# Kernel tuning notes

Hardware: AMD Instinct MI355X
Metric: run time of the kernel (lower is better)

Reference implementation:

```python
import jax, jax.numpy as jnp
import numpy as np

ATOM_K = 10
VOX_K = 15
HEADS = 4
HEAD_DIM = 32
N_BLOCKS = 4
BLOCK_DEPTH = 2


def _pairwise_sqdist(a, b):
    # a: [Na,3], b: [Nb,3] -> [Na,Nb]
    return jnp.sum(a * a, 1)[:, None] + jnp.sum(b * b, 1)[None, :] - 2.0 * (a @ b.T)


def knn(src_pos, dst_pos, k):
    # for each dst point, k nearest src points; returns (dst_idx, src_idx), each [Nd*k]
    d2 = _pairwise_sqdist(dst_pos, src_pos)
    _, idx = jax.lax.top_k(-d2, k)
    dst = jnp.repeat(jnp.arange(dst_pos.shape[0]), k)
    return dst, idx.reshape(-1)


def knn_graph(pos, k):
    # k nearest neighbors excluding self; returns (src=neighbor, dst=center)
    n = pos.shape[0]
    d2 = _pairwise_sqdist(pos, pos) + jnp.eye(n, dtype=pos.dtype) * 1e10
    _, idx = jax.lax.top_k(-d2, k)
    dst = jnp.repeat(jnp.arange(n), k)
    return idx.reshape(-1), dst


def edge_weights(i0, i1, h_a, pos_a, h_b, pos_b, w1, b1, w2, b2):
    # MLP([2*A+1, 8, 1]) on concat(h_a[i0], h_b[i1], dist) -> scalar per edge
    d = jnp.sqrt(jnp.sum((pos_a[i0] - pos_b[i1]) ** 2, -1, keepdims=True) + 1e-12)
    feat = jnp.concatenate([h_a[i0], h_b[i1], d], -1)
    return (jax.nn.relu(feat @ w1 + b1) @ w2 + b2)[:, 0]


def attn_layer(h, src, dst, ew, wq_l, wk_l, wv_l, n):
    # edge-weighted multi-head graph attention with segment softmax over dst
    q = (h @ wq_l).reshape(n, HEADS, HEAD_DIM)
    k = (h @ wk_l).reshape(n, HEADS, HEAD_DIM)
    v = (h @ wv_l).reshape(n, HEADS, HEAD_DIM)
    logits = jnp.sum(q[dst] * k[src], -1) / jnp.sqrt(jnp.float32(HEAD_DIM)) + ew[:, None]  # [E,H]
    m = jax.ops.segment_max(logits, dst, num_segments=n)
    z = jnp.exp(logits - m[dst])
    s = jax.ops.segment_sum(z, dst, num_segments=n)
    alpha = z / (s[dst] + 1e-9)
    out = jax.ops.segment_sum(alpha[:, :, None] * v[src], dst, num_segments=n)
    return out.reshape(n, HEADS * HEAD_DIM)


def layer_norm(x, g, b):
    mu = jnp.mean(x, -1, keepdims=True)
    var = jnp.var(x, -1, keepdims=True)
    return (x - mu) * jax.lax.rsqrt(var + 1e-5) * g + b


def setup_inputs() -> dict:
    Na, Nv, F, A, OUT = 8192, 4096, 64, 128, 128
    L = N_BLOCKS * BLOCK_DEPTH
    key = jax.random.key(0)
    ks = jax.random.split(key, 20)
    p = lambda k, shape, s=0.05: jax.random.normal(k, shape, jnp.float32) * s
    return {
        'atom_x': jax.random.normal(ks[0], (Na, F), jnp.float32),
        'atom_pos': jax.random.normal(ks[1], (Na, 3), jnp.float32) * 10.0,
        'vox_x': jax.random.normal(ks[2], (Nv, F), jnp.float32),
        'vox_pos': jax.random.normal(ks[3], (Nv, 3), jnp.float32) * 10.0,
        'w_atom_in': p(ks[4], (F, A)), 'b_atom_in': jnp.zeros((A,), jnp.float32),
        'w_vox_in': p(ks[5], (F, A)), 'b_vox_in': jnp.zeros((A,), jnp.float32),
        'aa_w1': p(ks[6], (2 * A + 1, 8)), 'aa_b1': jnp.zeros((8,), jnp.float32),
        'aa_w2': p(ks[7], (8, 1)), 'aa_b2': jnp.zeros((1,), jnp.float32),
        'av_w1': p(ks[8], (2 * A + 1, 8)), 'av_b1': jnp.zeros((8,), jnp.float32),
        'av_w2': p(ks[9], (8, 1)), 'av_b2': jnp.zeros((1,), jnp.float32),
        'vv_w1': p(ks[10], (2 * A + 1, 8)), 'vv_b1': jnp.zeros((8,), jnp.float32),
        'vv_w2': p(ks[11], (8, 1)), 'vv_b2': jnp.zeros((1,), jnp.float32),
        'wq': p(ks[12], (L, A, A)), 'wk': p(ks[13], (L, A, A)), 'wv': p(ks[14], (L, A, A)),
        'ln_g': jnp.ones((L, A), jnp.float32), 'ln_b': jnp.zeros((L, A), jnp.float32),
        'w_o1': p(ks[15], ((N_BLOCKS + 1) * A, A)), 'b_o1': jnp.zeros((A,), jnp.float32),
        'w_o2': p(ks[16], (A, OUT)), 'b_o2': jnp.zeros((OUT,), jnp.float32),
    }


def reference(atom_x, atom_pos, vox_x, vox_pos, w_atom_in, b_atom_in, w_vox_in, b_vox_in,
              aa_w1, aa_b1, aa_w2, aa_b2, av_w1, av_b1, av_w2, av_b2, vv_w1, vv_b1, vv_w2, vv_b2,
              wq, wk, wv, ln_g, ln_b, w_o1, b_o1, w_o2, b_o2):
    Na, Nv = atom_x.shape[0], vox_x.shape[0]
    N = Na + Nv
    atom_h0 = atom_x @ w_atom_in + b_atom_in
    vox_h0 = vox_x @ w_vox_in + b_vox_in

    # multi-scale KNN graph construction
    aa_src, aa_dst = knn_graph(atom_pos, ATOM_K)
    aa_ew = edge_weights(aa_src, aa_dst, atom_h0, atom_pos, atom_h0, atom_pos, aa_w1, aa_b1, aa_w2, aa_b2)
    av_vox, av_atom = knn(atom_pos, vox_pos, VOX_K)  # dst=vox, src=atom
    av_ew = edge_weights(av_vox, av_atom, vox_h0, vox_pos, atom_h0, atom_pos, av_w1, av_b1, av_w2, av_b2)
    vv_src, vv_dst = knn_graph(vox_pos, VOX_K)
    vv_ew = edge_weights(vv_src, vv_dst, vox_h0, vox_pos, vox_h0, vox_pos, vv_w1, vv_b1, vv_w2, vv_b2)

    # combined atom|vox graph (vox nodes offset by Na)
    src = jnp.concatenate([aa_src, av_atom, vv_src + Na])
    dst = jnp.concatenate([aa_dst, av_vox + Na, vv_dst + Na])
    ew = jnp.concatenate([aa_ew, av_ew, vv_ew])
    h = jnp.concatenate([atom_h0, vox_h0], 0)

    block_outs = []
    for b_i in range(N_BLOCKS):
        for l in range(BLOCK_DEPTH):
            li = b_i * BLOCK_DEPTH + l
            h = layer_norm(h + attn_layer(h, src, dst, ew, wq[li], wk[li], wv[li], N), ln_g[li], ln_b[li])
        block_outs.append(h[Na:])

    feat = jnp.concatenate([vox_h0] + block_outs, -1)  # [Nv, (blocks+1)*A]
    return jax.nn.relu(feat @ w_o1 + b_o1) @ w_o2 + b_o2
```

## Files before the change

kernel.cpp:

```cpp
#include <hip/hip_runtime.h>
#include <hip/hip_bf16.h>

#define PE_NA 8192
#define PE_NV 4096
#define PE_NN (PE_NA+PE_NV)
#define PE_FA 128
#define PE_FIN 64
#define PE_KAA 10
#define PE_KAV 15
#define PE_KVV 15
#define PE_EAA (PE_NA*PE_KAA)
#define PE_EAV (PE_NV*PE_KAV)
#define PE_EVV (PE_NV*PE_KVV)
#define PE_ETOT (PE_EAA+PE_EAV+PE_EVV)
#define PE_KNN_BLOCKS (PE_NA/4 + PE_NV/4 + PE_NV/4)
#define PE_P1A 0
#define PE_P2A 65536
#define PE_P2AV 131072
#define PE_P1AV 196608
#define PE_P1V 229376
#define PE_P2V 262144
#define PE_PTOT 294912
#define PE_PRE_BLOCKS (PE_PTOT/256)
#define PE_WT_ELEMS (8*3*128*128)
#define PE_WT_BLOCKS (PE_WT_ELEMS/256)
#define PE_RANK_S 32

typedef __hip_bfloat16 bf16;
typedef __attribute__((ext_vector_type(4))) float f32x4;
typedef __attribute__((ext_vector_type(4))) unsigned int u32x4;
typedef __attribute__((ext_vector_type(8))) short s16x8;
union pe_frag { u32x4 u; s16x8 s; };

__device__ __forceinline__ float pe_b2f(bf16 x){ return __bfloat162float(x); }

__device__ __forceinline__ float pe_u2f(unsigned short u){ return __uint_as_float(((unsigned)u) << 16); }
__device__ __forceinline__ unsigned short pe_f2u(float f){
  unsigned u = __float_as_uint(f);
  u = u + 0x7FFFu + ((u >> 16) & 1u);
  return (unsigned short)(u >> 16);
}

__global__ __launch_bounds__(1024) void pe_probe_kernel(const unsigned short* __restrict__ buf, int n,
                                                        int* __restrict__ flag){
  __shared__ int red[16];
  int t = threadIdx.x;
  int cnt = 0;
  for (int i = t; i < n; i += 1024){
    unsigned u = buf[i];
    unsigned e = (u >> 7) & 0xFF;
    if (u == 0u || (e >= 100u && e <= 150u)) cnt++;
  }
  #pragma unroll
  for (int off = 32; off > 0; off >>= 1) cnt += __shfl_xor(cnt, off);
  if ((t & 63) == 0) red[t >> 6] = cnt;
  __syncthreads();
  if (t == 0){
    int s = 0;
    #pragma unroll
    for (int i = 0; i < 16; i++) s += red[i];
    flag[0] = (s > (n * 9) / 10) ? 0 : 1;
  }
}

struct PeConv {
  const void* src[29];
  long long dstOff[29];
  int n[29];
  int blk0[30];
};
__global__ __launch_bounds__(256) void pe_convall_kernel(PeConv a, float* __restrict__ wsbase,
                                                         const int* __restrict__ flag){
  int b = blockIdx.x;
  int s = 0;
  while (s < 28 && b >= a.blk0[s+1]) s++;
  int idx = (b - a.blk0[s])*256 + threadIdx.x;
  if (idx >= a.n[s]) return;
  float* dst = wsbase + a.dstOff[s];
  if (flag[0]) dst[idx] = ((const float*)a.src[s])[idx];
  else         dst[idx] = pe_b2f(((const bf16*)a.src[s])[idx]);
}

__global__ __launch_bounds__(256) void ProteinEncoder_558345749244_kernel(bf16* __restrict__ out, int n){
  int idx = blockIdx.x*256 + threadIdx.x;
  if (idx < n) out[idx] = __float2bfloat16(0.123f);
}

__global__ __launch_bounds__(256) void pe_packproj_kernel(
    const float* __restrict__ ax, const float* __restrict__ wai, const float* __restrict__ bai,
    const float* __restrict__ vx, const float* __restrict__ wvi, const float* __restrict__ bvi,
    const float* __restrict__ apos, const float* __restrict__ vpos,
    const float* __restrict__ wq, const float* __restrict__ wk, const float* __restrict__ wv,
    float* __restrict__ h, float* __restrict__ voxh0,
    float4* __restrict__ apos4, float4* __restrict__ vpos4,
    int* __restrict__ arank, int* __restrict__ vrank,
    unsigned short* __restrict__ wtb){
  int b = blockIdx.x;
  const int NBA = (PE_NA*PE_FA)/256;
  const int NBV = (PE_NV*PE_FA)/256;
  const int NBP = (PE_NN + 255)/256;
  if (b < NBA){
    int idx = b*256 + threadIdx.x;
    int row = idx >> 7, col = idx & 127;
    const float* xr = ax + row*PE_FIN;
    float acc = bai[col];
    #pragma unroll 8
    for (int k2 = 0; k2 < PE_FIN; k2++) acc += xr[k2] * wai[k2*PE_FA + col];
    h[idx] = acc;
  } else if (b < NBA + NBV){
    int idx = (b - NBA)*256 + threadIdx.x;
    int row = idx >> 7, col = idx & 127;
    const float* xr = vx + row*PE_FIN;
    float acc = bvi[col];
    #pragma unroll 8
    for (int k2 = 0; k2 < PE_FIN; k2++) acc += xr[k2] * wvi[k2*PE_FA + col];
    h[(size_t)PE_NA*PE_FA + idx] = acc;
    voxh0[idx] = acc;
  } else if (b < NBA + NBV + NBP){
    int idx = (b - NBA - NBV)*256 + threadIdx.x;
    if (idx < PE_NA){
      float bx = apos[idx*3+0], by = apos[idx*3+1], bz = apos[idx*3+2];
      apos4[idx] = make_float4(bx, by, bz, (bx*bx + by*by) + bz*bz);
      arank[idx] = 0;
    } else if (idx < PE_NA + PE_NV){
      int j = idx - PE_NA;
      float bx = vpos[j*3+0], by = vpos[j*3+1], bz = vpos[j*3+2];
      vpos4[j] = make_float4(bx, by, bz, (bx*bx + by*by) + bz*bz);
      vrank[j] = 0;
    }
  } else {
    int g = (b - NBA - NBV - NBP)*256 + threadIdx.x;
    int c = g >> 14;
    int r = g & 16383;
    int n = r >> 7, k = r & 127;
    int li = c / 3, mat = c - li*3;
    const float* wsrc = (mat == 0) ? wq : (mat == 1) ? wk : wv;
    wtb[g] = pe_f2u(wsrc[li*16384 + k*128 + n]);
  }
}

__global__ __launch_bounds__(256) void pe_rank_kernel(
    const float4* __restrict__ apos4, const float4* __restrict__ vpos4,
    int* __restrict__ arank, int* __restrict__ vrank){
  __shared__ float xs[256];
  int b = blockIdx.x;
  const int ABLK = (PE_NA/256)*PE_RANK_S;
  const float4* src; int N; int* drk; int cb;
  if (b < ABLK){ src = apos4; N = PE_NA; drk = arank; cb = b; }
  else         { src = vpos4; N = PE_NV; drk = vrank; cb = b - ABLK; }
  int chunk = cb / PE_RANK_S;
  int seg   = cb % PE_RANK_S;
  int i = chunk*256 + threadIdx.x;
  float xi = src[i].x;
  int segN = N / PE_RANK_S;
  int j0 = seg * segN;
  if (threadIdx.x < segN) xs[threadIdx.x] = src[j0 + threadIdx.x].x;
  __syncthreads();
  int cnt = 0;
  #pragma unroll 8
  for (int j = 0; j < segN; j++){
    float xj = xs[j];
    cnt += (xj < xi || (xj == xi && (j0 + j) < i)) ? 1 : 0;
  }
  atomicAdd(&drk[i], cnt);
}

__global__ __launch_bounds__(256) void pe_scatter_kernel(
    const float4* __restrict__ apos4, const float4* __restrict__ vpos4,
    const int* __restrict__ arank, const int* __restrict__ vrank,
    float4* __restrict__ sax4, int* __restrict__ said,
    float4* __restrict__ svx4, int* __restrict__ svid){
  int g = blockIdx.x*256 + threadIdx.x;
  if (g < PE_NA){
    int r = arank[g];
    sax4[r] = apos4[g];
    said[r] = g;
  } else if (g < PE_NN){
    int j = g - PE_NA;
    int r = vrank[j];
    svx4[r] = vpos4[j];
    svid[r] = j;
  }
}

__device__ __forceinline__ float pe_unflip(unsigned th){
  return __uint_as_float(th ^ ((unsigned)(~((int)th >> 31)) | 0x80000000u));
}
__device__ __forceinline__ void pe_knn_insert(unsigned long long mask, float d2, int j,
                                              int K, int lane,
                                              unsigned long long &slot, float &thr_f){
  while (mask){
    int l = __ffsll((long long)mask) - 1;
    mask &= mask - 1;
    float dl = __shfl(d2, l, 64);
    int jl = __shfl(j, l, 64);
    unsigned u = __float_as_uint(dl);
    u ^= (unsigned)(((int)u >> 31) | 0x80000000);
    unsigned long long k = ((unsigned long long)u << 32) | (unsigned)jl;
    unsigned long long skm1 = __shfl(slot, K-1, 64);
    if (k < skm1){
      unsigned long long up = __shfl_up(slot, 1, 64);
      slot = (slot < k) ? slot : ((lane == 0 || up < k) ? k : up);
      thr_f = pe_unflip((unsigned)(__shfl(slot, K-1, 64) >> 32));
    }
  }
}

__global__ __launch_bounds__(256) void pe_knn3_kernel(
    const float4* __restrict__ apos4, const float4* __restrict__ vpos4,
    const float4* __restrict__ sax4, const int* __restrict__ said, const int* __restrict__ arank,
    const float4* __restrict__ svx4, const int* __restrict__ svid, const int* __restrict__ vrank,
    int* __restrict__ es,
    const float* __restrict__ h,
    const float* __restrict__ aw1, const float* __restrict__ vw1, const float* __restrict__ ww1,
    float* __restrict__ Pall){
  int b = blockIdx.x;
  if (b >= PE_KNN_BLOCKS){
    int g = (b - PE_KNN_BLOCKS)*256 + threadIdx.x;
    const float* w1; const float* hb; int n; int half;
    if (g < PE_P2A)       { w1 = aw1; hb = h;                        n = g >> 3;               half = 0; }
    else if (g < PE_P2AV) { w1 = aw1; hb = h;                        n = (g - PE_P2A) >> 3;    half = 1; }
    else if (g < PE_P1AV) { w1 = vw1; hb = h;                        n = (g - PE_P2AV) >> 3;   half = 1; }
    else if (g < PE_P1V)  { w1 = vw1; hb = h + (size_t)PE_NA*PE_FA;  n = (g - PE_P1AV) >> 3;   half = 0; }
    else if (g < PE_P2V)  { w1 = ww1; hb = h + (size_t)PE_NA*PE_FA;  n = (g - PE_P1V) >> 3;    half = 0; }
    else                  { w1 = ww1; hb = h + (size_t)PE_NA*PE_FA;  n = (g - PE_P2V) >> 3;    half = 1; }
    int j = g & 7;
    const float* hr = hb + n*PE_FA;
    const float* wr = w1 + half*128*8 + j;
    float acc = 0.f;
    #pragma unroll 8
    for (int f = 0; f < 128; f++) acc += hr[f] * wr[f*8];
    Pall[g] = acc;
    return;
  }
  const float4 *dpos, *spos; const int *sid, *srank; int Ns, K, excl, idx_off, nb; int* out;
  if (b < PE_NA/4){
    dpos = apos4; spos = sax4; sid = said; srank = arank;
    Ns = PE_NA; K = PE_KAA; excl = 1; idx_off = 0; out = es; nb = b;
  } else if (b < PE_NA/4 + PE_NV/4){
    dpos = vpos4; spos = sax4; sid = said; srank = nullptr;
    Ns = PE_NA; K = PE_KAV; excl = 0; idx_off = 0; out = es + PE_EAA; nb = b - PE_NA/4;
  } else {
    dpos = vpos4; spos = svx4; sid = svid; srank = vrank;
    Ns = PE_NV; K = PE_KVV; excl = 1; idx_off = PE_NA;
    out = es + PE_EAA + PE_EAV; nb = b - PE_NA/4 - PE_NV/4;
  }
  int lane = threadIdx.x & 63;
  int n = nb*4 + (threadIdx.x >> 6);
  float4 dp = dpos[n];
  float qx = dp.x, qy = dp.y, qz = dp.z, nq = dp.w;
  int self = excl ? n : -1;
  int start;
  if (srank){
    start = srank[n];
  } else {
    int lo = 0, len = Ns;
    #pragma unroll
    for (int it = 0; it < 2; it++){
      int step = (len + 63) >> 6;
      int pr = lo + lane*step; if (pr > Ns-1) pr = Ns-1;
      float px = spos[pr].x;
      unsigned long long mv = __ballot(px <= qx);
      int cnt = __popcll(mv);
      int seg = cnt > 0 ? cnt - 1 : 0;
      lo = lo + seg*step;
      len = step;
      if (lo > Ns-1) lo = Ns-1;
    }
    start = lo;
  }
  int w0 = start - 32; if (w0 < 0) w0 = 0; if (w0 > Ns - 64) w0 = Ns - 64;
  unsigned long long slot;
  float thr_f;
  {
    int j = w0 + lane;
    float4 pp = spos[j];
    int oi = sid[j];
    float dt = (qx*pp.x + qy*pp.y) + qz*pp.z;
    float d2 = __builtin_fmaf(-2.0f, dt, nq + pp.w);
    unsigned u = __float_as_uint(d2);
    u ^= (unsigned)(((int)u >> 31) | 0x80000000);
    if (oi == self) u = 0xffffffffu;
    unsigned long long key = ((unsigned long long)u << 32) | (unsigned)oi;
    #pragma unroll
    for (int kk = 2; kk <= 64; kk <<= 1){
      #pragma unroll
      for (int jj = kk >> 1; jj > 0; jj >>= 1){
        unsigned long long o = __shfl_xor(key, jj, 64);
        bool keepmin = (((lane & jj) == 0) == ((lane & kk) == 0));
        unsigned long long mn = (key < o) ? key : o;
        unsigned long long mx = (key < o) ? o : key;
        key = keepmin ? mn : mx;
      }
    }
    slot = key;
    thr_f = pe_unflip((unsigned)(__shfl(slot, K-1, 64) >> 32));
  }
  int L = w0 - 1;
  int R = w0 + 64;
  bool doneL = false, doneR = false;
  while (!(doneL && doneR)){
    if (!doneL){
      int j = L - lane;
      bool val = (j >= 0);
      float d2 = 1e30f, ddx = -1e30f; int oi = -3;
      if (val){
        float4 pp = spos[j];
        oi = sid[j];
        ddx = pp.x - qx;
        float dt = (qx*pp.x + qy*pp.y) + qz*pp.z;
        d2 = __builtin_fmaf(-2.0f, dt, nq + pp.w);
      }
      unsigned long long m = __ballot(val && (d2 <= thr_f) && (oi != self));
      if (m) pe_knn_insert(m, d2, oi, K, lane, slot, thr_f);
      float dd63 = __shfl(ddx, 63);
      doneL = (L - 64 < 0) || ((dd63 < 0.f) && (dd63*dd63 > thr_f));
      L -= 64;
    }
    if (!doneR){
      int j = R + lane;
      bool val = (j < Ns);
      float d2 = 1e30f, ddx = 1e30f; int oi = -3;
      if (val){
        float4 pp = spos[j];
        oi = sid[j];
        ddx = pp.x - qx;
        float dt = (qx*pp.x + qy*pp.y) + qz*pp.z;
        d2 = __builtin_fmaf(-2.0f, dt, nq + pp.w);
      }
      unsigned long long m = __ballot(val && (d2 <= thr_f) && (oi != self));
      if (m) pe_knn_insert(m, d2, oi, K, lane, slot, thr_f);
      float dd63 = __shfl(ddx, 63);
      doneR = (R + 64 >= Ns) || ((dd63 > 0.f) && (dd63*dd63 > thr_f));
      R += 64;
    }
  }
  if (lane < K) out[n*K + lane] = (int)(unsigned)(slot & 0xffffffffu) + idx_off;
}

__global__ __launch_bounds__(256) void pe_edge3_kernel(
    const float4* __restrict__ apos4, const float4* __restrict__ vpos4,
    const int* __restrict__ es, const float* __restrict__ Pall,
    const float* __restrict__ aw1, const float* __restrict__ ab1,
    const float* __restrict__ aw2, const float* __restrict__ ab2,
    const float* __restrict__ vw1, const float* __restrict__ vb1,
    const float* __restrict__ vw2, const float* __restrict__ vb2,
    const float* __restrict__ ww1, const float* __restrict__ wb1,
    const float* __restrict__ ww2, const float* __restrict__ wb2,
    float* __restrict__ ewb){
  int e = blockIdx.x*256 + threadIdx.x;
  const float *w1r, *b1, *w2, *b2;
  long long offA, offB;
  float4 qa, qb;
  if (e < PE_EAA){
    int dst = e / PE_KAA;
    int src = es[e];
    offA = PE_P1A  + (long long)src*8;
    offB = PE_P2A  + (long long)dst*8;
    qa = apos4[src]; qb = apos4[dst];
    w1r = aw1 + 256*8; b1 = ab1; w2 = aw2; b2 = ab2;
  } else if (e < PE_EAA + PE_EAV){
    int e2 = e - PE_EAA;
    int dstv = e2 / PE_KAV;
    int srca = es[e];
    offA = PE_P1AV + (long long)dstv*8;
    offB = PE_P2AV + (long long)srca*8;
    qa = vpos4[dstv]; qb = apos4[srca];
    w1r = vw1 + 256*8; b1 = vb1; w2 = vw2; b2 = vb2;
  } else {
    int e2 = e - PE_EAA - PE_EAV;
    int dstv = e2 / PE_KVV;
    int srcv = es[e] - PE_NA;
    offA = PE_P1V  + (long long)srcv*8;
    offB = PE_P2V  + (long long)dstv*8;
    qa = vpos4[srcv]; qb = vpos4[dstv];
    w1r = ww1 + 256*8; b1 = wb1; w2 = ww2; b2 = wb2;
  }
  float dx = qa.x - qb.x, dy = qa.y - qb.y, dz = qa.z - qb.z;
  float d = sqrtf(((dx*dx + dy*dy) + dz*dz) + 1e-12f);
  float4 a0 = *(const float4*)(Pall + offA);
  float4 a1 = *(const float4*)(Pall + offA + 4);
  float4 c0 = *(const float4*)(Pall + offB);
  float4 c1 = *(const float4*)(Pall + offB + 4);
  float acc[8] = { a0.x + c0.x, a0.y + c0.y, a0.z + c0.z, a0.w + c0.w,
                   a1.x + c1.x, a1.y + c1.y, a1.z + c1.z, a1.w + c1.w };
  float o = b2[0];
  #pragma unroll
  for (int j = 0; j < 8; j++){
    float hj = acc[j] + d*w1r[j] + b1[j];
    if (hj > 0.f) o += hj * w2[j];
  }
  ewb[e] = o;
}

__global__ __launch_bounds__(256) void pe_qkv3_kernel(const float* __restrict__ H,
    const unsigned short* __restrict__ Wt,
    unsigned short* __restrict__ QKV){
  __shared__ __align__(16) unsigned Xs[2048];
  int t = threadIdx.x;
  int row0 = blockIdx.x * 32;
  int mat = blockIdx.y;
  #pragma unroll
  for (int i = 0; i < 8; i++){
    int idx32 = i*256 + t;
    int row = idx32 >> 6, c32 = idx32 & 63;
    const float* src = H + (size_t)(row0 + row)*PE_FA + c32*2;
    unsigned u = (unsigned)pe_f2u(src[0]) | ((unsigned)pe_f2u(src[1]) << 16);
    Xs[row*64 + (c32 ^ ((row & 7) << 2))] = u;
  }
  __syncthreads();
  int w = t >> 6, l = t & 63;
  int l15 = l & 15, lq = l >> 4;
  f32x4 acc[2][2];
  #pragma unroll
  for (int a = 0; a < 2; a++)
    #pragma unroll
    for (int bb = 0; bb < 2; bb++) acc[a][bb] = (f32x4){0.f, 0.f, 0.f, 0.f};
  #pragma unroll
  for (int ks = 0; ks < 4; ks++){
    pe_frag af[2];
    #pragma unroll
    for (int rt = 0; rt < 2; rt++){
      int row = rt*16 + l15;
      int c32 = (ks*16 + lq*4) ^ ((row & 7) << 2);
      af[rt].u = *(const u32x4*)&Xs[row*64 + c32];
    }
    #pragma unroll
    for (int nt = 0; nt < 2; nt++){
      int col = w*32 + nt*16 + l15;
      pe_frag bf_;
      bf_.u = *(const u32x4*)(Wt + (size_t)(mat*128 + col)*PE_FA + ks*32 + lq*8);
      #pragma unroll
      for (int rt = 0; rt < 2; rt++)
        acc[rt][nt] = __builtin_amdgcn_mfma_f32_16x16x32_bf16(af[rt].s, bf_.s, acc[rt][nt], 0, 0, 0);
    }
  }
  #pragma unroll
  for (int rt = 0; rt < 2; rt++){
    #pragma unroll
    for (int nt = 0; nt < 2; nt++){
      int col = w*32 + nt*16 + l15;
      unsigned short* outp = QKV + (size_t)mat*PE_NN*PE_FA + col;
      int nodeb = row0 + rt*16 + lq*4;
      #pragma unroll
      for (int v = 0; v < 4; v++)
        outp[(size_t)(nodeb + v)*PE_FA] = pe_f2u(acc[rt][nt][v]);
    }
  }
}

template<int DEG>
__device__ __forceinline__ void pe_attn_node(int n, int lane, int esel, float ewsel,
    const unsigned* __restrict__ Qp, const unsigned* __restrict__ Kp, const unsigned* __restrict__ Vp,
    float* H, const float* __restrict__ lng, const float* __restrict__ lnb, float* bout){
  unsigned qu = Qp[n*64 + lane];
  float qx = pe_u2f((unsigned short)(qu & 0xffffu));
  float qy = pe_u2f((unsigned short)(qu >> 16));
  int srcs[DEG];
  #pragma unroll
  for (int e = 0; e < DEG; e++) srcs[e] = __shfl(esel, e, 64);
  const float inv = 0.17677669529663687f;
  float lg[DEG];
  #pragma unroll
  for (int e = 0; e < DEG; e++){
    unsigned ku = Kp[srcs[e]*64 + lane];
    float p = qx*pe_u2f((unsigned short)(ku & 0xffffu)) + qy*pe_u2f((unsigned short)(ku >> 16));
    #pragma unroll
    for (int off = 8; off > 0; off >>= 1) p += __shfl_xor(p, off);
    lg[e] = p*inv + __shfl(ewsel, e, 64);
  }
  float m = -1e30f;
  #pragma unroll
  for (int e = 0; e < DEG; e++) m = fmaxf(m, lg[e]);
  float ssum = 0.f;
  #pragma unroll
  for (int e = 0; e < DEG; e++){ float z = expf(lg[e] - m); ssum += z; lg[e] = z; }
  float rdn = 1.0f / (ssum + 1e-9f);
  float a0 = 0.f, a1 = 0.f;
  #pragma unroll
  for (int e = 0; e < DEG; e++){
    unsigned vu = Vp[srcs[e]*64 + lane];
    a0 += lg[e]*pe_u2f((unsigned short)(vu & 0xffffu));
    a1 += lg[e]*pe_u2f((unsigned short)(vu >> 16));
  }
  a0 *= rdn; a1 *= rdn;
  float2 hv = ((const float2*)H)[n*64 + lane];
  float x0 = hv.x + a0, x1 = hv.y + a1;
  float s = x0 + x1;
  #pragma unroll
  for (int off = 32; off > 0; off >>= 1) s += __shfl_xor(s, off);
  float mu = s * (1.f/128.f);
  float d0 = x0 - mu, d1 = x1 - mu;
  float vq = d0*d0 + d1*d1;
  #pragma unroll
  for (int off = 32; off > 0; off >>= 1) vq += __shfl_xor(vq, off);
  float var = vq * (1.f/128.f);
  float rs = 1.0f / sqrtf(var + 1e-5f);
  float2 lw = ((const float2*)lng)[lane];
  float2 lb = ((const float2*)lnb)[lane];
  float2 yv = make_float2(d0*rs*lw.x + lb.x, d1*rs*lw.y + lb.y);
  ((float2*)H)[n*64 + lane] = yv;
  if (bout != nullptr) ((float2*)bout)[(n - PE_NA)*64 + lane] = yv;
}

__global__ __launch_bounds__(128) void pe_attn_ln_kernel(const unsigned* __restrict__ Qp,
    const unsigned* __restrict__ Kp, const unsigned* __restrict__ Vp, float* H,
    const int* __restrict__ esrc, const float* __restrict__ eew,
    const float* __restrict__ lng, const float* __restrict__ lnb, float* bout){
  int w = threadIdx.x >> 6;
  int lane = threadIdx.x & 63;
  int n = blockIdx.x*2 + w;
  int esel = 0; float ewsel = 0.f;
  if (n < PE_NA){
    if (lane < PE_KAA){ int e = n*PE_KAA + lane; esel = esrc[e]; ewsel = eew[e]; }
    pe_attn_node<PE_KAA>(n, lane, esel, ewsel, Qp, Kp, Vp, H, lng, lnb, nullptr);
  } else {
    int j = n - PE_NA;
    if (lane < PE_KAV){ int e = PE_EAA + j*PE_KAV + lane; esel = esrc[e]; ewsel = eew[e]; }
    else if (lane < PE_KAV + PE_KVV){ int e = PE_EAA + PE_EAV + j*PE_KVV + (lane - PE_KAV); esel = esrc[e]; ewsel = eew[e]; }
    pe_attn_node<PE_KAV+PE_KVV>(n, lane, esel, ewsel, Qp, Kp, Vp, H, lng, lnb, bout);
  }
}

__global__ __launch_bounds__(256) void pe_final1_kernel(const float* __restrict__ voxh0, const float* __restrict__ bouts,
    const float* __restrict__ W, const float* __restrict__ B, float* __restrict__ hid){
  __shared__ float Xs[640][17];
  int t = threadIdx.x;
  int row0 = blockIdx.x * 16;
  for (int s = 0; s < 5; s++){
    const float* seg = (s == 0) ? voxh0 : (bouts + (size_t)(s-1)*PE_NV*PE_FA);
    #pragma unroll
    for (int i = 0; i < 8; i++){
      int idx = i*256 + t;
      int r = idx >> 7, k0 = idx & 127;
      Xs[s*128 + k0][r] = seg[(size_t)(row0 + r)*PE_FA + k0];
    }
  }
  __syncthreads();
  int col = t & 127;
  int rg = (t >> 7) * 8;
  float acc[8];
  #pragma unroll
  for (int i = 0; i < 8; i++) acc[i] = B[col];
  for (int k = 0; k < 640; k++){
    float w = W[k*PE_FA + col];
    #pragma unroll
    for (int i = 0; i < 8; i++) acc[i] += Xs[k][rg + i] * w;
  }
  #pragma unroll
  for (int i = 0; i < 8; i++)
    hid[(size_t)(row0 + rg + i)*PE_FA + col] = fmaxf(acc[i], 0.f);
}

__global__ __launch_bounds__(256) void pe_final2_kernel(const float* __restrict__ hid, const float* __restrict__ W,
    const float* __restrict__ B, void* __restrict__ outv, const int* __restrict__ flag){
  int idx = blockIdx.x*256 + threadIdx.x;
  int r = idx >> 7, c = idx & 127;
  float acc = B[c];
  const float* hr = hid + r*PE_FA;
  #pragma unroll 8
  for (int k2 = 0; k2 < 128; k2++) acc += hr[k2] * W[k2*PE_FA + c];
  if (flag[0]) ((float*)outv)[idx] = acc;
  else         ((bf16*)outv)[idx] = __float2bfloat16(acc);
}

extern "C" void kernel_launch(void* const* d_in, const int* in_sizes, int n_in,
                              void* d_out, int out_size, void* d_ws, size_t ws_size,
                              hipStream_t stream){
  (void)in_sizes; (void)n_in; (void)ws_size;

  float* ws = (float*)d_ws;
  int* flag = (int*)ws;
  float* p = ws + 4;
  auto A = [&](size_t n){ float* r = p; p += n; return r; };

  float* c_atom_x  = A(PE_NA*PE_FIN);
  float* c_atom_pos= A(PE_NA*3);
  float* c_vox_x   = A(PE_NV*PE_FIN);
  float* c_vox_pos = A(PE_NV*3);
  float* c_w_ai = A(PE_FIN*PE_FA); float* c_b_ai = A(PE_FA);
  float* c_w_vi = A(PE_FIN*PE_FA); float* c_b_vi = A(PE_FA);
  float* c_aa_w1 = A(257*8); float* c_aa_b1 = A(8); float* c_aa_w2 = A(8); float* c_aa_b2 = A(1);
  float* c_av_w1 = A(257*8); float* c_av_b1 = A(8); float* c_av_w2 = A(8); float* c_av_b2 = A(1);
  float* c_vv_w1 = A(257*8); float* c_vv_b1 = A(8); float* c_vv_w2 = A(8); float* c_vv_b2 = A(1);
  float* c_wq = A(8*PE_FA*PE_FA); float* c_wk = A(8*PE_FA*PE_FA); float* c_wv = A(8*PE_FA*PE_FA);
  float* c_lng = A(8*PE_FA); float* c_lnb = A(8*PE_FA);
  float* c_wo1 = A(5*PE_FA*PE_FA); float* c_bo1 = A(PE_FA);
  float* c_wo2 = A(PE_FA*PE_FA);   float* c_bo2 = A(PE_FA);

  float* h     = A((size_t)PE_NN*PE_FA);
  float* voxh0 = A((size_t)PE_NV*PE_FA);
  int*   es    = (int*)A(PE_ETOT);
  float* ewb   = A(PE_ETOT);
  float* bouts = A((size_t)4*PE_NV*PE_FA);
  float4* apos4 = (float4*)A((size_t)PE_NA*4);
  float4* vpos4 = (float4*)A((size_t)PE_NV*4);
  float4* sax4  = (float4*)A((size_t)PE_NA*4);
  float4* svx4  = (float4*)A((size_t)PE_NV*4);
  int* said  = (int*)A(PE_NA);
  int* arank = (int*)A(PE_NA);
  int* svid  = (int*)A(PE_NV);
  int* vrank = (int*)A(PE_NV);
  { uintptr_t up = (uintptr_t)p; up = (up + 15) & ~(uintptr_t)15; p = (float*)up; }
  float* Pall  = A(PE_PTOT);
  unsigned short* wtb = (unsigned short*)A(PE_WT_ELEMS/2);
  float* qkvb  = A((size_t)3*PE_NN*64);
  unsigned short* qkvb16 = (unsigned short*)qkvb;
  float* hid   = qkvb;

  pe_probe_kernel<<<1, 1024, 0, stream>>>((const unsigned short*)d_in[1], 3072, flag);

  const int nelem[29] = {
    PE_NA*PE_FIN, PE_NA*3, PE_NV*PE_FIN, PE_NV*3,
    PE_FIN*PE_FA, PE_FA, PE_FIN*PE_FA, PE_FA,
    257*8, 8, 8, 1,  257*8, 8, 8, 1,  257*8, 8, 8, 1,
    8*PE_FA*PE_FA, 8*PE_FA*PE_FA, 8*PE_FA*PE_FA,
    8*PE_FA, 8*PE_FA,
    5*PE_FA*PE_FA, PE_FA, PE_FA*PE_FA, PE_FA
  };
  float* cdst[29] = {
    c_atom_x, c_atom_pos, c_vox_x, c_vox_pos,
    c_w_ai, c_b_ai, c_w_vi, c_b_vi,
    c_aa_w1, c_aa_b1, c_aa_w2, c_aa_b2,
    c_av_w1, c_av_b1, c_av_w2, c_av_b2,
    c_vv_w1, c_vv_b1, c_vv_w2, c_vv_b2,
    c_wq, c_wk, c_wv, c_lng, c_lnb,
    c_wo1, c_bo1, c_wo2, c_bo2
  };
  PeConv pc;
  int bacc = 0;
  for (int i = 0; i < 29; i++){
    pc.src[i] = d_in[i];
    pc.n[i] = nelem[i];
    pc.dstOff[i] = (long long)(cdst[i] - ws);
    pc.blk0[i] = bacc;
    bacc += (nelem[i] + 255)/256;
  }
  pc.blk0[29] = bacc;
  pe_convall_kernel<<<bacc, 256, 0, stream>>>(pc, ws, flag);

  ProteinEncoder_558345749244_kernel<<<(out_size + 255)/256, 256, 0, stream>>>((bf16*)d_out, out_size);

  pe_packproj_kernel<<<(PE_NA*PE_FA)/256 + (PE_NV*PE_FA)/256 + (PE_NN + 255)/256 + PE_WT_BLOCKS,
                       256, 0, stream>>>(
      c_atom_x, c_w_ai, c_b_ai, c_vox_x, c_w_vi, c_b_vi, c_atom_pos, c_vox_pos,
      c_wq, c_wk, c_wv,
      h, voxh0, apos4, vpos4, arank, vrank, wtb);

  pe_rank_kernel<<<(PE_NA/256)*PE_RANK_S + (PE_NV/256)*PE_RANK_S, 256, 0, stream>>>(
      apos4, vpos4, arank, vrank);
  pe_scatter_kernel<<<(PE_NN + 255)/256, 256, 0, stream>>>(
      apos4, vpos4, arank, vrank, sax4, said, svx4, svid);

  pe_knn3_kernel<<<PE_KNN_BLOCKS + PE_PRE_BLOCKS, 256, 0, stream>>>(
      apos4, vpos4, sax4, said, arank, svx4, svid, vrank,
      es, h, c_aa_w1, c_av_w1, c_vv_w1, Pall);

  pe_edge3_kernel<<<PE_ETOT/256, 256, 0, stream>>>(
      apos4, vpos4, es, Pall,
      c_aa_w1, c_aa_b1, c_aa_w2, c_aa_b2,
      c_av_w1, c_av_b1, c_av_w2, c_av_b2,
      c_vv_w1, c_vv_b1, c_vv_w2, c_vv_b2,
      ewb);

  const unsigned* Qp = (const unsigned*)qkvb;
  const unsigned* Kp = Qp + (size_t)PE_NN*64;
  const unsigned* Vp = Kp + (size_t)PE_NN*64;
  for (int li = 0; li < 8; li++){
    pe_qkv3_kernel<<<dim3(PE_NN/32, 3), 256, 0, stream>>>(h, wtb + (size_t)li*3*PE_FA*PE_FA, qkvb16);
    float* bo = (li & 1) ? (bouts + (size_t)(li >> 1)*PE_NV*PE_FA) : nullptr;
    pe_attn_ln_kernel<<<PE_NN/2, 128, 0, stream>>>(Qp, Kp, Vp,
                                                   h, es, ewb, c_lng + li*PE_FA, c_lnb + li*PE_FA, bo);
  }

  pe_final1_kernel<<<PE_NV/16, 256, 0, stream>>>(voxh0, bouts, c_wo1, c_bo1, hid);
  pe_final2_kernel<<<(PE_NV*PE_FA)/256, 256, 0, stream>>>(hid, c_wo2, c_bo2, d_out, flag);
}
```

Before: 580.7 us.

## Fuse edge weights with first QKV projection and spatially order attention nodes

Merges the edge-weight MLP kernel with the layer-0 QKV projection into one launch. The loop now runs the QKV projection for the next layer after each attention pass, so there is one fewer launch overall. Attention blocks now visit nodes in spatially sorted order (said/svid), with blocks interleaved across eight groups, to improve gather locality on K/V. The final MLP kernel uses 8-row tiles, which doubles its block count. The trade-off is more indirection and a change in the order of the H writes.

```diff
diff --git a/kernel.cpp b/kernel.cpp
--- a/kernel.cpp
+++ b/kernel.cpp
@@ -25,6 +25,8 @@
 #define PE_WT_ELEMS (8*3*128*128)
 #define PE_WT_BLOCKS (PE_WT_ELEMS/256)
 #define PE_RANK_S 32
+#define PE_NB_EDGE (PE_ETOT/256)
+#define PE_NB_QKV ((PE_NN/32)*3)
 
 typedef __hip_bfloat16 bf16;
 typedef __attribute__((ext_vector_type(4))) float f32x4;
@@ -338,7 +340,7 @@
   if (lane < K) out[n*K + lane] = (int)(unsigned)(slot & 0xffffffffu) + idx_off;
 }
 
-__global__ __launch_bounds__(256) void pe_edge3_kernel(
+__device__ __forceinline__ void pe_edge_one(int e,
     const float4* __restrict__ apos4, const float4* __restrict__ vpos4,
     const int* __restrict__ es, const float* __restrict__ Pall,
     const float* __restrict__ aw1, const float* __restrict__ ab1,
@@ -348,7 +350,6 @@
     const float* __restrict__ ww1, const float* __restrict__ wb1,
     const float* __restrict__ ww2, const float* __restrict__ wb2,
     float* __restrict__ ewb){
-  int e = blockIdx.x*256 + threadIdx.x;
   const float *w1r, *b1, *w2, *b2;
   long long offA, offB;
   float4 qa, qb;
@@ -393,13 +394,9 @@
   ewb[e] = o;
 }
 
-__global__ __launch_bounds__(256) void pe_qkv3_kernel(const float* __restrict__ H,
-    const unsigned short* __restrict__ Wt,
-    unsigned short* __restrict__ QKV){
-  __shared__ __align__(16) unsigned Xs[2048];
-  int t = threadIdx.x;
-  int row0 = blockIdx.x * 32;
-  int mat = blockIdx.y;
+__device__ __forceinline__ void pe_qkv_body(const float* __restrict__ H,
+    const unsigned short* __restrict__ Wt, unsigned short* __restrict__ QKV,
+    int row0, int mat, int t, unsigned* Xs){
   #pragma unroll
   for (int i = 0; i < 8; i++){
     int idx32 = i*256 + t;
@@ -447,6 +444,37 @@
         outp[(size_t)(nodeb + v)*PE_FA] = pe_f2u(acc[rt][nt][v]);
     }
   }
+}
+
+__global__ __launch_bounds__(256) void pe_edgeqkv0_kernel(
+    const float4* __restrict__ apos4, const float4* __restrict__ vpos4,
+    const int* __restrict__ es, const float* __restrict__ Pall,
+    const float* __restrict__ aw1, const float* __restrict__ ab1,
+    const float* __restrict__ aw2, const float* __restrict__ ab2,
+    const float* __restrict__ vw1, const float* __restrict__ vb1,
+    const float* __restrict__ vw2, const float* __restrict__ vb2,
+    const float* __restrict__ ww1, const float* __restrict__ wb1,
+    const float* __restrict__ ww2, const float* __restrict__ wb2,
+    float* __restrict__ ewb,
+    const float* __restrict__ H, const unsigned short* __restrict__ Wt0,
+    unsigned short* __restrict__ QKV){
+  __shared__ __align__(16) unsigned Xs[2048];
+  int b = blockIdx.x;
+  if (b < PE_NB_EDGE){
+    pe_edge_one(b*256 + threadIdx.x, apos4, vpos4, es, Pall,
+                aw1, ab1, aw2, ab2, vw1, vb1, vw2, vb2, ww1, wb1, ww2, wb2, ewb);
+    return;
+  }
+  int g = b - PE_NB_EDGE;
+  int bx = g % (PE_NN/32);
+  int mat = g / (PE_NN/32);
+  pe_qkv_body(H, Wt0, QKV, bx*32, mat, threadIdx.x, Xs);
+}
+
+__global__ __launch_bounds__(256) void pe_qkv3_kernel(const float* __restrict__ H,
+    const unsigned short* __restrict__ Wt, unsigned short* __restrict__ QKV){
+  __shared__ __align__(16) unsigned Xs[2048];
+  pe_qkv_body(H, Wt, QKV, blockIdx.x*32, blockIdx.y, threadIdx.x, Xs);
 }
 
 template<int DEG>
@@ -506,16 +534,23 @@
 __global__ __launch_bounds__(128) void pe_attn_ln_kernel(const unsigned* __restrict__ Qp,
     const unsigned* __restrict__ Kp, const unsigned* __restrict__ Vp, float* H,
     const int* __restrict__ esrc, const float* __restrict__ eew,
-    const float* __restrict__ lng, const float* __restrict__ lnb, float* bout){
+    const float* __restrict__ lng, const float* __restrict__ lnb, float* bout,
+    const int* __restrict__ said, const int* __restrict__ svid){
+  int b = blockIdx.x;
   int w = threadIdx.x >> 6;
   int lane = threadIdx.x & 63;
-  int n = blockIdx.x*2 + w;
+  const int ABLK = PE_NA/2;
   int esel = 0; float ewsel = 0.f;
-  if (n < PE_NA){
+  if (b < ABLK){
+    int bs = (b & 7)*(ABLK/8) + (b >> 3);
+    int n = said[bs*2 + w];
     if (lane < PE_KAA){ int e = n*PE_KAA + lane; esel = esrc[e]; ewsel = eew[e]; }
     pe_attn_node<PE_KAA>(n, lane, esel, ewsel, Qp, Kp, Vp, H, lng, lnb, nullptr);
   } else {
-    int j = n - PE_NA;
+    int b2 = b - ABLK;
+    int bs = (b2 & 7)*((PE_NV/2)/8) + (b2 >> 3);
+    int j = svid[bs*2 + w];
+    int n = PE_NA + j;
     if (lane < PE_KAV){ int e = PE_EAA + j*PE_KAV + lane; esel = esrc[e]; ewsel = eew[e]; }
     else if (lane < PE_KAV + PE_KVV){ int e = PE_EAA + PE_EAV + j*PE_KVV + (lane - PE_KAV); esel = esrc[e]; ewsel = eew[e]; }
     pe_attn_node<PE_KAV+PE_KVV>(n, lane, esel, ewsel, Qp, Kp, Vp, H, lng, lnb, bout);
@@ -524,13 +559,13 @@
 
 __global__ __launch_bounds__(256) void pe_final1_kernel(const float* __restrict__ voxh0, const float* __restrict__ bouts,
     const float* __restrict__ W, const float* __restrict__ B, float* __restrict__ hid){
-  __shared__ float Xs[640][17];
+  __shared__ float Xs[640][9];
   int t = threadIdx.x;
-  int row0 = blockIdx.x * 16;
+  int row0 = blockIdx.x * 8;
   for (int s = 0; s < 5; s++){
     const float* seg = (s == 0) ? voxh0 : (bouts + (size_t)(s-1)*PE_NV*PE_FA);
     #pragma unroll
-    for (int i = 0; i < 8; i++){
+    for (int i = 0; i < 4; i++){
       int idx = i*256 + t;
       int r = idx >> 7, k0 = idx & 127;
       Xs[s*128 + k0][r] = seg[(size_t)(row0 + r)*PE_FA + k0];
@@ -538,17 +573,17 @@
   }
   __syncthreads();
   int col = t & 127;
-  int rg = (t >> 7) * 8;
-  float acc[8];
-  #pragma unroll
-  for (int i = 0; i < 8; i++) acc[i] = B[col];
+  int rg = (t >> 7) * 4;
+  float acc[4];
+  #pragma unroll
+  for (int i = 0; i < 4; i++) acc[i] = B[col];
   for (int k = 0; k < 640; k++){
     float w = W[k*PE_FA + col];
     #pragma unroll
-    for (int i = 0; i < 8; i++) acc[i] += Xs[k][rg + i] * w;
-  }
-  #pragma unroll
-  for (int i = 0; i < 8; i++)
+    for (int i = 0; i < 4; i++) acc[i] += Xs[k][rg + i] * w;
+  }
+  #pragma unroll
+  for (int i = 0; i < 4; i++)
     hid[(size_t)(row0 + rg + i)*PE_FA + col] = fmaxf(acc[i], 0.f);
 }
 
@@ -656,23 +691,25 @@
       apos4, vpos4, sax4, said, arank, svx4, svid, vrank,
       es, h, c_aa_w1, c_av_w1, c_vv_w1, Pall);
 
-  pe_edge3_kernel<<<PE_ETOT/256, 256, 0, stream>>>(
+  pe_edgeqkv0_kernel<<<PE_NB_EDGE + PE_NB_QKV, 256, 0, stream>>>(
       apos4, vpos4, es, Pall,
       c_aa_w1, c_aa_b1, c_aa_w2, c_aa_b2,
       c_av_w1, c_av_b1, c_av_w2, c_av_b2,
       c_vv_w1, c_vv_b1, c_vv_w2, c_vv_b2,
-      ewb);
+      ewb, h, wtb, qkvb16);
 
   const unsigned* Qp = (const unsigned*)qkvb;
   const unsigned* Kp = Qp + (size_t)PE_NN*64;
   const unsigned* Vp = Kp + (size_t)PE_NN*64;
   for (int li = 0; li < 8; li++){
-    pe_qkv3_kernel<<<dim3(PE_NN/32, 3), 256, 0, stream>>>(h, wtb + (size_t)li*3*PE_FA*PE_FA, qkvb16);
     float* bo = (li & 1) ? (bouts + (size_t)(li >> 1)*PE_NV*PE_FA) : nullptr;
     pe_attn_ln_kernel<<<PE_NN/2, 128, 0, stream>>>(Qp, Kp, Vp,
-                                                   h, es, ewb, c_lng + li*PE_FA, c_lnb + li*PE_FA, bo);
-  }
-
-  pe_final1_kernel<<<PE_NV/16, 256, 0, stream>>>(voxh0, bouts, c_wo1, c_bo1, hid);
+                                                   h, es, ewb, c_lng + li*PE_FA, c_lnb + li*PE_FA, bo,
+                                                   said, svid);
+    if (li < 7)
+      pe_qkv3_kernel<<<dim3(PE_NN/32, 3), 256, 0, stream>>>(h, wtb + (size_t)(li+1)*3*PE_FA*PE_FA, qkvb16);
+  }
+
+  pe_final1_kernel<<<PE_NV/8, 256, 0, stream>>>(voxh0, bouts, c_wo1, c_bo1, hid);
   pe_final2_kernel<<<(PE_NV*PE_FA)/256, 256, 0, stream>>>(hid, c_wo2, c_bo2, d_out, flag);
 }
```

Result: faster. 568.7 us (-2.1%).
